# Performance work log

Measured on AMD Instinct MI355X. Metric: run time of the kernel, lower is better.

## Reference

```python
import jax, jax.numpy as jnp
import numpy as np

NEG_INF = jnp.finfo(jnp.float32).min

def setup_inputs() -> dict:
    key = jax.random.key(0)
    k1, k2, k3, k4 = jax.random.split(key, 4)
    B, H, S, DK, DV = 2, 16, 2048, 64, 64
    Q = jax.random.normal(k1, (B, H, S, DK), dtype=jnp.float32)
    K = jax.random.normal(k2, (B, H, S, DK), dtype=jnp.float32)
    V = jax.random.normal(k3, (B, H, S, DV), dtype=jnp.float32)
    mask = jax.random.randint(k4, (B, 1, S, S), 0, 2, dtype=jnp.int32)
    return {"Q": Q, "K": K, "V": V, "mask": mask}

def reference(Q, K, V, mask):
    d_k = Q.shape[-1]
    # scores: [B, H, Sq, Sk]
    scores = jnp.einsum('bhqd,bhkd->bhqk', Q, K) / jnp.sqrt(jnp.float32(d_k))
    scores = jnp.where(mask == 0, NEG_INF, scores)
    attn_weights = jax.nn.softmax(scores, axis=-1)
    # dropout p=0.0 -> identity (eval-mode reference)
    output = jnp.einsum('bhqk,bhkv->bhqv', attn_weights, V)
    return (output, attn_weights)
```

## Files before the change

### kernel.cpp

```cpp
#include <hip/hip_runtime.h>


typedef __attribute__((ext_vector_type(4))) float f32x4;
typedef __attribute__((ext_vector_type(8))) short s16x8;
typedef __attribute__((ext_vector_type(4))) unsigned short u16x4;
typedef __attribute__((ext_vector_type(8))) unsigned short u16x8;
typedef __attribute__((ext_vector_type(4))) unsigned int u32x4;

#define S_LEN 2048
#define D_DIM 64
#define H_NUM 16
#define B_NUM 2
#define NT    32
#define SW    32
#define QSCALE 0.18033688011112042f

__device__ __forceinline__ int swz(int row, int colByte) {
  return row * 128 + (colByte ^ ((row & 7) << 4));
}

__device__ __forceinline__ unsigned short f2bf(float f) {
  unsigned int x = __builtin_bit_cast(unsigned int, f);
  x = (x + 0x7FFFu + ((x >> 16) & 1u)) >> 16;
  return (unsigned short)x;
}

__device__ __forceinline__ unsigned cvt_pk_bf16(float lo, float hi) {
  unsigned r;
  asm("v_cvt_pk_bf16_f32 %0, %1, %2" : "=v"(r) : "v"(lo), "v"(hi));
  return r;
}

__device__ __forceinline__ f32x4 mfma16(f32x4 acc, s16x8 a, s16x8 b) {
  return __builtin_amdgcn_mfma_f32_16x16x32_bf16(a, b, acc, 0, 0, 0);
}


__global__ __launch_bounds__(256) void prep_kernel(
    const float* __restrict__ Q, const float* __restrict__ K,
    const float* __restrict__ V, const int* __restrict__ m,
    u16x4* __restrict__ Q16, u16x4* __restrict__ K16,
    unsigned short* __restrict__ VT, unsigned long long* __restrict__ bits)
{
  const int blk = blockIdx.x;
  const int tid = threadIdx.x;

  if (blk < 1024) {
    __shared__ unsigned short t[64][72];
    const int bh = blk >> 5;
    const int st = blk & 31;
    const float* src = V + ((size_t)bh * S_LEN + st * 64) * D_DIM;
    const int r0 = tid >> 4;
    const int c  = (tid & 15) * 4;
#pragma unroll
    for (int i = 0; i < 4; ++i) {
      const int r = r0 + i * 16;
      float4 v = *(const float4*)(src + r * D_DIM + c);
      t[c + 0][r] = f2bf(v.x); t[c + 1][r] = f2bf(v.y);
      t[c + 2][r] = f2bf(v.z); t[c + 3][r] = f2bf(v.w);
    }
    __syncthreads();
#pragma unroll
    for (int i = 0; i < 4; ++i) {
      const int idx = tid + i * 256;
      const int d  = idx >> 4;
      const int t0 = (idx & 15) * 4;
      const int sp = ((t0 >> 5) & 1) * 32 + ((t0 & 7) >> 2) * 16 + ((t0 >> 3) & 3) * 4;
      u16x4 o = *(const u16x4*)&t[d][sp];
      *(u16x4*)(VT + ((size_t)bh * D_DIM + d) * S_LEN + st * 64 + t0) = o;
    }
  } else if (blk < 2048) {
    const int n4 = B_NUM * H_NUM * S_LEN * D_DIM / 4;
    const int step = 1024 * 256;
    for (int i = (blk - 1024) * 256 + tid; i < n4; i += step) {
      float4 q = ((const float4*)Q)[i];
      Q16[i] = u16x4{f2bf(q.x * QSCALE), f2bf(q.y * QSCALE),
                     f2bf(q.z * QSCALE), f2bf(q.w * QSCALE)};
      float4 k = ((const float4*)K)[i];
      K16[i] = u16x4{f2bf(k.x), f2bf(k.y), f2bf(k.z), f2bf(k.w)};
    }
  } else {
    const int total = B_NUM * S_LEN * S_LEN;
    const int step  = 1024 * 256;
    for (int i = (blk - 2048) * 256 + tid; i < total; i += step) {
      unsigned long long b = __ballot(m[i] != 0);
      if ((tid & 63) == 0) bits[i >> 6] = b;
    }
  }
}


__global__ __launch_bounds__(256) void attn_rowsum_kernel(
    const unsigned short* __restrict__ Q16, const unsigned short* __restrict__ K16,
    const unsigned long long* __restrict__ Mb, float* __restrict__ lpq)
{
  const int tid  = threadIdx.x;
  const int lane = tid & 63;
  const int wv   = tid >> 6;
  const int l15  = lane & 15;
  const int g4   = lane >> 4;

  const int wg = blockIdx.x;
  const int lg = (wg & 7) * 128 + (wg >> 3);
  const int qt = lg & 31;
  const int bh = lg >> 5;
  const int b  = bh >> 4;

  __shared__ __align__(16) char Kbuf[16384];

  const unsigned short* Qg16 = Q16 + ((size_t)bh * S_LEN + qt * 64 + wv * 16 + l15) * D_DIM + g4 * 8;
  const unsigned short* Kg16 = K16 + (size_t)bh * S_LEN * D_DIM;
  float* lpg = lpq + (size_t)bh * S_LEN + qt * 64;
  const unsigned long long* Mg = Mb + ((size_t)b * S_LEN + qt * 64) * SW;

  const s16x8 qa0 = *(const s16x8*)Qg16;
  const s16x8 qa1 = *(const s16x8*)(Qg16 + 32);

  float lps = 0.f;

  const int sr  = tid >> 3;
  const int ss  = tid & 7;
  const int ssb = ss * 16;

  {
    u16x8 k0 = *(const u16x8*)(Kg16 + (size_t)sr * D_DIM + ss * 8);
    u16x8 k1 = *(const u16x8*)(Kg16 + (size_t)(sr + 32) * D_DIM + ss * 8);
    *(u16x8*)(Kbuf + swz(sr, ssb))      = k0;
    *(u16x8*)(Kbuf + swz(sr + 32, ssb)) = k1;
  }
  __syncthreads();

  int cur = 0;
  for (int kt = 0; kt < NT; ++kt) {
    const int ktn = (kt + 1 < NT) ? kt + 1 : kt;
    u16x8 kr0 = *(const u16x8*)(Kg16 + (size_t)(ktn * 64 + sr) * D_DIM + ss * 8);
    u16x8 kr1 = *(const u16x8*)(Kg16 + (size_t)(ktn * 64 + sr + 32) * D_DIM + ss * 8);
    __builtin_amdgcn_sched_barrier(0);

    char* Kc = Kbuf + cur * 8192;
    const unsigned long long mw = Mg[(wv * 16 + l15) * SW + kt];

    f32x4 sacc[4];
#pragma unroll
    for (int i = 0; i < 4; ++i) sacc[i] = f32x4{0.f, 0.f, 0.f, 0.f};
#pragma unroll
    for (int ct = 0; ct < 4; ++ct) {
      s16x8 b0 = *(const s16x8*)(Kc + swz(ct * 16 + l15, g4 * 16));
      s16x8 b1 = *(const s16x8*)(Kc + swz(ct * 16 + l15, g4 * 16 + 64));
      sacc[ct] = mfma16(sacc[ct], b0, qa0);
      sacc[ct] = mfma16(sacc[ct], b1, qa1);
    }

#pragma unroll
    for (int ct = 0; ct < 4; ++ct) {
#pragma unroll
      for (int r = 0; r < 4; ++r) {
        float e = __builtin_amdgcn_exp2f(sacc[ct][r]);
        lps += ((mw >> (ct * 16 + g4 * 4 + r)) & 1ull) ? e : 0.f;
      }
    }

    char* Kn = Kbuf + (cur ^ 1) * 8192;
    *(u16x8*)(Kn + swz(sr, ssb))      = kr0;
    *(u16x8*)(Kn + swz(sr + 32, ssb)) = kr1;
    __syncthreads();
    cur ^= 1;
  }

  lps += __shfl_xor(lps, 16);
  lps += __shfl_xor(lps, 32);
  if (g4 == 0) lpg[wv * 16 + l15] = 1.0f / lps;
}


__global__ __launch_bounds__(256) void attn_main_kernel(
    const unsigned short* __restrict__ Q16, const unsigned short* __restrict__ K16,
    const unsigned short* __restrict__ VT16, const unsigned long long* __restrict__ Mb,
    const float* __restrict__ lpq, float* __restrict__ Op, float* __restrict__ Wp)
{
  const int tid  = threadIdx.x;
  const int lane = tid & 63;
  const int wv   = tid >> 6;
  const int l15  = lane & 15;
  const int g4   = lane >> 4;

  const int wg = blockIdx.x;
  const int lg = (wg & 7) * 128 + (wg >> 3);
  const int qt = lg & 31;
  const int bh = lg >> 5;
  const int b  = bh >> 4;

  __shared__ __align__(16) char lds[32768];
  char* Kbuf = lds;
  char* Vbuf = lds + 16384;

  const unsigned short* Qg16 = Q16 + ((size_t)bh * S_LEN + qt * 64 + wv * 16 + l15) * D_DIM + g4 * 8;
  const unsigned short* Kg16 = K16 + (size_t)bh * S_LEN * D_DIM;
  const unsigned short* Vg   = VT16 + (size_t)bh * D_DIM * S_LEN;
  float* Og = Op + ((size_t)bh * S_LEN + qt * 64) * D_DIM;
  float* Wrow = Wp + ((size_t)bh * S_LEN + qt * 64 + wv * 16 + l15) * S_LEN;
  const unsigned long long* Mg = Mb + ((size_t)b * S_LEN + qt * 64) * SW;
  const float* lpg = lpq + (size_t)bh * S_LEN + qt * 64;

  const s16x8 qa0 = *(const s16x8*)Qg16;
  const s16x8 qa1 = *(const s16x8*)(Qg16 + 32);

  const float lpr = lpg[wv * 16 + l15];
  float lpn[4];
#pragma unroll
  for (int r = 0; r < 4; ++r) lpn[r] = lpg[wv * 16 + g4 * 4 + r];

  f32x4 oacc[4];
#pragma unroll
  for (int i = 0; i < 4; ++i) oacc[i] = f32x4{0.f, 0.f, 0.f, 0.f};

  const int sr  = tid >> 3;
  const int ss  = tid & 7;
  const int ssb = ss * 16;

  {
    u16x8 k0 = *(const u16x8*)(Kg16 + (size_t)sr * D_DIM + ss * 8);
    u16x8 k1 = *(const u16x8*)(Kg16 + (size_t)(sr + 32) * D_DIM + ss * 8);
    u16x8 v0 = *(const u16x8*)(Vg + (size_t)sr * S_LEN + ss * 8);
    u16x8 v1 = *(const u16x8*)(Vg + (size_t)(sr + 32) * S_LEN + ss * 8);
    *(u16x8*)(Kbuf + swz(sr, ssb))      = k0;
    *(u16x8*)(Kbuf + swz(sr + 32, ssb)) = k1;
    *(u16x8*)(Vbuf + swz(sr, ssb))      = v0;
    *(u16x8*)(Vbuf + swz(sr + 32, ssb)) = v1;
  }
  __syncthreads();

  int cur = 0;
  for (int kt = 0; kt < NT; ++kt) {
    const int ktn = (kt + 1 < NT) ? kt + 1 : kt;
    u16x8 kr0 = *(const u16x8*)(Kg16 + (size_t)(ktn * 64 + sr) * D_DIM + ss * 8);
    u16x8 kr1 = *(const u16x8*)(Kg16 + (size_t)(ktn * 64 + sr + 32) * D_DIM + ss * 8);
    u16x8 vr0 = *(const u16x8*)(Vg + (size_t)sr * S_LEN + ktn * 64 + ss * 8);
    u16x8 vr1 = *(const u16x8*)(Vg + (size_t)(sr + 32) * S_LEN + ktn * 64 + ss * 8);
    __builtin_amdgcn_sched_barrier(0);

    char* Kc = Kbuf + cur * 8192;
    char* Vc = Vbuf + cur * 8192;

    const unsigned long long mw = Mg[(wv * 16 + l15) * SW + kt];

    f32x4 sacc[4];
#pragma unroll
    for (int i = 0; i < 4; ++i) sacc[i] = f32x4{0.f, 0.f, 0.f, 0.f};
#pragma unroll
    for (int ct = 0; ct < 4; ++ct) {
      s16x8 b0 = *(const s16x8*)(Kc + swz(ct * 16 + l15, g4 * 16));
      s16x8 b1 = *(const s16x8*)(Kc + swz(ct * 16 + l15, g4 * 16 + 64));
      sacc[ct] = mfma16(sacc[ct], b0, qa0);
      sacc[ct] = mfma16(sacc[ct], b1, qa1);
    }

    unsigned pw[8];
#pragma unroll
    for (int ct = 0; ct < 4; ++ct) {
      float e0 = __builtin_amdgcn_exp2f(sacc[ct][0]);
      float e1 = __builtin_amdgcn_exp2f(sacc[ct][1]);
      float e2 = __builtin_amdgcn_exp2f(sacc[ct][2]);
      float e3 = __builtin_amdgcn_exp2f(sacc[ct][3]);
      e0 = ((mw >> (ct * 16 + g4 * 4 + 0)) & 1ull) ? e0 : 0.f;
      e1 = ((mw >> (ct * 16 + g4 * 4 + 1)) & 1ull) ? e1 : 0.f;
      e2 = ((mw >> (ct * 16 + g4 * 4 + 2)) & 1ull) ? e2 : 0.f;
      e3 = ((mw >> (ct * 16 + g4 * 4 + 3)) & 1ull) ? e3 : 0.f;
      f32x4 w = {e0 * lpr, e1 * lpr, e2 * lpr, e3 * lpr};
      __builtin_nontemporal_store(w,
          (f32x4*)(Wrow + (size_t)kt * 64 + ct * 16 + g4 * 4));
      pw[2 * ct]     = cvt_pk_bf16(e0, e1);
      pw[2 * ct + 1] = cvt_pk_bf16(e2, e3);
    }
    const s16x8 pa0 = __builtin_bit_cast(s16x8, u32x4{pw[0], pw[1], pw[2], pw[3]});
    const s16x8 pa1 = __builtin_bit_cast(s16x8, u32x4{pw[4], pw[5], pw[6], pw[7]});

#pragma unroll
    for (int ct = 0; ct < 4; ++ct) {
      s16x8 v0 = *(const s16x8*)(Vc + swz(ct * 16 + l15, g4 * 16));
      s16x8 v1 = *(const s16x8*)(Vc + swz(ct * 16 + l15, g4 * 16 + 64));
      oacc[ct] = mfma16(oacc[ct], pa0, v0);
      oacc[ct] = mfma16(oacc[ct], pa1, v1);
    }

    char* Kn = Kbuf + (cur ^ 1) * 8192;
    char* Vn = Vbuf + (cur ^ 1) * 8192;
    *(u16x8*)(Kn + swz(sr, ssb))      = kr0;
    *(u16x8*)(Kn + swz(sr + 32, ssb)) = kr1;
    *(u16x8*)(Vn + swz(sr, ssb))      = vr0;
    *(u16x8*)(Vn + swz(sr + 32, ssb)) = vr1;
    __syncthreads();
    cur ^= 1;
  }

#pragma unroll
  for (int ct = 0; ct < 4; ++ct)
#pragma unroll
    for (int r = 0; r < 4; ++r)
      Og[(size_t)(wv * 16 + g4 * 4 + r) * D_DIM + ct * 16 + l15] = oacc[ct][r] * lpn[r];
}


__global__ __launch_bounds__(256) void attn_fwd_kernel(
    const float* __restrict__ Qp, const float* __restrict__ Kp, const float* __restrict__ Vp,
    const int* __restrict__ Mi, float* __restrict__ Op, float* __restrict__ Wp)
{
  const int tid  = threadIdx.x;
  const int lane = tid & 63;
  const int wv   = tid >> 6;
  const int l15  = lane & 15;
  const int g4   = lane >> 4;

  const int wg = blockIdx.x;
  const int lg = (wg & 7) * 128 + (wg >> 3);
  const int qt = lg & 31;
  const int bh = lg >> 5;
  const int b  = bh >> 4;

  __shared__ __align__(16) char lds[32768];
  char* Qs  = lds;
  char* Ks  = lds + 8192;
  char* VTs = lds + 16384;
  char* Ps  = lds + 24576 + (wv << 11);

  const float* Qg = Qp + ((size_t)bh * S_LEN + qt * 64) * D_DIM;
  const float* Kg = Kp + (size_t)bh * S_LEN * D_DIM;
  const float* Vg = Vp + (size_t)bh * S_LEN * D_DIM;
  float* Og = Op + ((size_t)bh * S_LEN + qt * 64) * D_DIM;
  float* Wg = Wp + ((size_t)bh * S_LEN + qt * 64) * S_LEN;
  const int* Mig = Mi + ((size_t)b * S_LEN + qt * 64) * S_LEN;

  {
    const int r0 = tid >> 4;
    const int c  = (tid & 15) * 4;
#pragma unroll
    for (int i = 0; i < 4; ++i) {
      const int r = r0 + i * 16;
      float4 v = *(const float4*)(Qg + r * D_DIM + c);
      ushort4 p; p.x = f2bf(v.x); p.y = f2bf(v.y); p.z = f2bf(v.z); p.w = f2bf(v.w);
      *(ushort4*)(Qs + swz(r, c * 2)) = p;
    }
  }
  __syncthreads();
  const s16x8 qa0 = *(const s16x8*)(Qs + swz(wv * 16 + l15, g4 * 16));
  const s16x8 qa1 = *(const s16x8*)(Qs + swz(wv * 16 + l15, g4 * 16 + 64));

  f32x4 oacc[4];
#pragma unroll
  for (int i = 0; i < 4; ++i) oacc[i] = f32x4{0.f, 0.f, 0.f, 0.f};
  float lp[4] = {0.f, 0.f, 0.f, 0.f};

  const int qrow = wv * 16 + g4 * 4;

  for (int kt = 0; kt < NT; ++kt) {
    __syncthreads();
    {
      const int r0 = tid >> 4;
      const int c  = (tid & 15) * 4;
      const float* Kt = Kg + kt * 64 * D_DIM;
#pragma unroll
      for (int i = 0; i < 4; ++i) {
        const int r = r0 + i * 16;
        float4 v = *(const float4*)(Kt + r * D_DIM + c);
        ushort4 p; p.x = f2bf(v.x); p.y = f2bf(v.y); p.z = f2bf(v.z); p.w = f2bf(v.w);
        *(ushort4*)(Ks + swz(r, c * 2)) = p;
      }
      const float* Vt = Vg + kt * 64 * D_DIM;
#pragma unroll
      for (int i = 0; i < 2; ++i) {
        const int rr = (tid >> 4) * 2 + i * 32;
        float4 a  = *(const float4*)(Vt + rr * D_DIM + c);
        float4 bq = *(const float4*)(Vt + (rr + 1) * D_DIM + c);
        const float av[4] = {a.x, a.y, a.z, a.w};
        const float bv[4] = {bq.x, bq.y, bq.z, bq.w};
#pragma unroll
        for (int j = 0; j < 4; ++j) {
          unsigned pk = (unsigned)f2bf(av[j]) | ((unsigned)f2bf(bv[j]) << 16);
          *(unsigned*)(VTs + swz(c + j, rr * 2)) = pk;
        }
      }
    }
    __syncthreads();

    f32x4 sacc[4];
#pragma unroll
    for (int i = 0; i < 4; ++i) sacc[i] = f32x4{0.f, 0.f, 0.f, 0.f};
#pragma unroll
    for (int ct = 0; ct < 4; ++ct) {
      s16x8 b0 = *(const s16x8*)(Ks + swz(ct * 16 + l15, g4 * 16));
      s16x8 b1 = *(const s16x8*)(Ks + swz(ct * 16 + l15, g4 * 16 + 64));
      sacc[ct] = mfma16(sacc[ct], qa0, b0);
      sacc[ct] = mfma16(sacc[ct], qa1, b1);
    }

#pragma unroll
    for (int ct = 0; ct < 4; ++ct) {
#pragma unroll
      for (int r = 0; r < 4; ++r) {
        float e = __expf(sacc[ct][r] * 0.125f);
        bool keep = Mig[(size_t)(qrow + r) * S_LEN + kt * 64 + ct * 16 + l15] != 0;
        e = keep ? e : 0.f;
        lp[r] += e;
        *(unsigned short*)(Ps + swz(g4 * 4 + r, (ct * 16 + l15) * 2)) = f2bf(e);
      }
    }
    asm volatile("s_waitcnt lgkmcnt(0)" ::: "memory");
    __builtin_amdgcn_sched_barrier(0);

    const s16x8 pa0 = *(const s16x8*)(Ps + swz(l15, g4 * 16));
    const s16x8 pa1 = *(const s16x8*)(Ps + swz(l15, g4 * 16 + 64));
#pragma unroll
    for (int ct = 0; ct < 4; ++ct) {
      s16x8 v0 = *(const s16x8*)(VTs + swz(ct * 16 + l15, g4 * 16));
      s16x8 v1 = *(const s16x8*)(VTs + swz(ct * 16 + l15, g4 * 16 + 64));
      oacc[ct] = mfma16(oacc[ct], pa0, v0);
      oacc[ct] = mfma16(oacc[ct], pa1, v1);
    }
  }

#pragma unroll
  for (int r = 0; r < 4; ++r) {
    float v = lp[r];
    v += __shfl_xor(v, 1);
    v += __shfl_xor(v, 2);
    v += __shfl_xor(v, 4);
    v += __shfl_xor(v, 8);
    lp[r] = 1.0f / v;
  }

#pragma unroll
  for (int ct = 0; ct < 4; ++ct)
#pragma unroll
    for (int r = 0; r < 4; ++r)
      Og[(size_t)(qrow + r) * D_DIM + ct * 16 + l15] = oacc[ct][r] * lp[r];

  for (int kt = 0; kt < NT; ++kt) {
    __syncthreads();
    {
      const int r0 = tid >> 4;
      const int c  = (tid & 15) * 4;
      const float* Kt = Kg + kt * 64 * D_DIM;
#pragma unroll
      for (int i = 0; i < 4; ++i) {
        const int r = r0 + i * 16;
        float4 v = *(const float4*)(Kt + r * D_DIM + c);
        ushort4 p; p.x = f2bf(v.x); p.y = f2bf(v.y); p.z = f2bf(v.z); p.w = f2bf(v.w);
        *(ushort4*)(Ks + swz(r, c * 2)) = p;
      }
    }
    __syncthreads();

    f32x4 sacc[4];
#pragma unroll
    for (int i = 0; i < 4; ++i) sacc[i] = f32x4{0.f, 0.f, 0.f, 0.f};
#pragma unroll
    for (int ct = 0; ct < 4; ++ct) {
      s16x8 b0 = *(const s16x8*)(Ks + swz(ct * 16 + l15, g4 * 16));
      s16x8 b1 = *(const s16x8*)(Ks + swz(ct * 16 + l15, g4 * 16 + 64));
      sacc[ct] = mfma16(sacc[ct], qa0, b0);
      sacc[ct] = mfma16(sacc[ct], qa1, b1);
    }

#pragma unroll
    for (int ct = 0; ct < 4; ++ct) {
#pragma unroll
      for (int r = 0; r < 4; ++r) {
        float e = __expf(sacc[ct][r] * 0.125f);
        bool keep = Mig[(size_t)(qrow + r) * S_LEN + kt * 64 + ct * 16 + l15] != 0;
        e = keep ? e : 0.f;
        __builtin_nontemporal_store(e * lp[r],
            Wg + (size_t)(qrow + r) * S_LEN + kt * 64 + ct * 16 + l15);
      }
    }
  }
}

extern "C" void kernel_launch(void* const* d_in, const int* in_sizes, int n_in,
                              void* d_out, int out_size, void* d_ws, size_t ws_size,
                              hipStream_t stream) {
  (void)in_sizes; (void)n_in; (void)out_size;
  const float* Q   = (const float*)d_in[0];
  const float* K   = (const float*)d_in[1];
  const float* V   = (const float*)d_in[2];
  const int* mask  = (const int*)d_in[3];
  float* Out = (float*)d_out;
  float* W   = Out + (size_t)B_NUM * H_NUM * S_LEN * D_DIM;

  const size_t bits_bytes = (size_t)(B_NUM * S_LEN * S_LEN / 64) * 8;
  const size_t t16_bytes  = (size_t)B_NUM * H_NUM * S_LEN * D_DIM * 2;
  const size_t lp_bytes   = (size_t)B_NUM * H_NUM * S_LEN * 4;
  unsigned long long* bits = (unsigned long long*)d_ws;

  if (ws_size >= bits_bytes + 3 * t16_bytes + lp_bytes) {
    unsigned short* Q16 = (unsigned short*)((char*)d_ws + bits_bytes);
    unsigned short* K16 = Q16 + t16_bytes / 2;
    unsigned short* VT  = K16 + t16_bytes / 2;
    float* lpq = (float*)((char*)d_ws + bits_bytes + 3 * t16_bytes);
    prep_kernel<<<3072, 256, 0, stream>>>(Q, K, V, mask,
                                          (u16x4*)Q16, (u16x4*)K16, VT, bits);
    attn_rowsum_kernel<<<1024, 256, 0, stream>>>(Q16, K16, bits, lpq);
    attn_main_kernel<<<1024, 256, 0, stream>>>(Q16, K16, VT, bits, lpq, Out, W);
  } else {
    attn_fwd_kernel<<<1024, 256, 0, stream>>>(Q, K, V, mask, Out, W);
  }
}
```

Before: 230.2 us.

## Share K/V tiles across two query tiles with 512-thread blocks in main kernel

```diff
diff --git a/kernel.cpp b/kernel.cpp
--- a/kernel.cpp
+++ b/kernel.cpp
@@ -173,7 +173,7 @@
 }
 
 
-__global__ __launch_bounds__(256) void attn_main_kernel(
+__global__ __launch_bounds__(512, 4) void attn_main_kernel(
     const unsigned short* __restrict__ Q16, const unsigned short* __restrict__ K16,
     const unsigned short* __restrict__ VT16, const unsigned long long* __restrict__ Mb,
     const float* __restrict__ lpq, float* __restrict__ Op, float* __restrict__ Wp)
@@ -183,32 +183,34 @@
   const int wv   = tid >> 6;
   const int l15  = lane & 15;
   const int g4   = lane >> 4;
+  const int wt   = wv & 3;
 
   const int wg = blockIdx.x;
-  const int lg = (wg & 7) * 128 + (wg >> 3);
-  const int qt = lg & 31;
-  const int bh = lg >> 5;
+  const int lg = (wg & 7) * 64 + (wg >> 3);
+  const int tp = lg & 15;
+  const int bh = lg >> 4;
   const int b  = bh >> 4;
+  const int qt = tp * 2 + (wv >> 2);
 
   __shared__ __align__(16) char lds[32768];
   char* Kbuf = lds;
   char* Vbuf = lds + 16384;
 
-  const unsigned short* Qg16 = Q16 + ((size_t)bh * S_LEN + qt * 64 + wv * 16 + l15) * D_DIM + g4 * 8;
+  const unsigned short* Qg16 = Q16 + ((size_t)bh * S_LEN + qt * 64 + wt * 16 + l15) * D_DIM + g4 * 8;
   const unsigned short* Kg16 = K16 + (size_t)bh * S_LEN * D_DIM;
   const unsigned short* Vg   = VT16 + (size_t)bh * D_DIM * S_LEN;
   float* Og = Op + ((size_t)bh * S_LEN + qt * 64) * D_DIM;
-  float* Wrow = Wp + ((size_t)bh * S_LEN + qt * 64 + wv * 16 + l15) * S_LEN;
-  const unsigned long long* Mg = Mb + ((size_t)b * S_LEN + qt * 64) * SW;
+  float* Wrow = Wp + ((size_t)bh * S_LEN + qt * 64 + wt * 16 + l15) * S_LEN;
+  const unsigned long long* Mrow = Mb + ((size_t)b * S_LEN + qt * 64 + wt * 16 + l15) * SW;
   const float* lpg = lpq + (size_t)bh * S_LEN + qt * 64;
 
   const s16x8 qa0 = *(const s16x8*)Qg16;
   const s16x8 qa1 = *(const s16x8*)(Qg16 + 32);
 
-  const float lpr = lpg[wv * 16 + l15];
+  const float lpr = lpg[wt * 16 + l15];
   float lpn[4];
 #pragma unroll
-  for (int r = 0; r < 4; ++r) lpn[r] = lpg[wv * 16 + g4 * 4 + r];
+  for (int r = 0; r < 4; ++r) lpn[r] = lpg[wt * 16 + g4 * 4 + r];
 
   f32x4 oacc[4];
 #pragma unroll
@@ -220,29 +222,23 @@
 
   {
     u16x8 k0 = *(const u16x8*)(Kg16 + (size_t)sr * D_DIM + ss * 8);
-    u16x8 k1 = *(const u16x8*)(Kg16 + (size_t)(sr + 32) * D_DIM + ss * 8);
     u16x8 v0 = *(const u16x8*)(Vg + (size_t)sr * S_LEN + ss * 8);
-    u16x8 v1 = *(const u16x8*)(Vg + (size_t)(sr + 32) * S_LEN + ss * 8);
-    *(u16x8*)(Kbuf + swz(sr, ssb))      = k0;
-    *(u16x8*)(Kbuf + swz(sr + 32, ssb)) = k1;
-    *(u16x8*)(Vbuf + swz(sr, ssb))      = v0;
-    *(u16x8*)(Vbuf + swz(sr + 32, ssb)) = v1;
+    *(u16x8*)(Kbuf + swz(sr, ssb)) = k0;
+    *(u16x8*)(Vbuf + swz(sr, ssb)) = v0;
   }
   __syncthreads();
 
   int cur = 0;
   for (int kt = 0; kt < NT; ++kt) {
     const int ktn = (kt + 1 < NT) ? kt + 1 : kt;
-    u16x8 kr0 = *(const u16x8*)(Kg16 + (size_t)(ktn * 64 + sr) * D_DIM + ss * 8);
-    u16x8 kr1 = *(const u16x8*)(Kg16 + (size_t)(ktn * 64 + sr + 32) * D_DIM + ss * 8);
-    u16x8 vr0 = *(const u16x8*)(Vg + (size_t)sr * S_LEN + ktn * 64 + ss * 8);
-    u16x8 vr1 = *(const u16x8*)(Vg + (size_t)(sr + 32) * S_LEN + ktn * 64 + ss * 8);
+    u16x8 kr = *(const u16x8*)(Kg16 + (size_t)(ktn * 64 + sr) * D_DIM + ss * 8);
+    u16x8 vr = *(const u16x8*)(Vg + (size_t)sr * S_LEN + ktn * 64 + ss * 8);
     __builtin_amdgcn_sched_barrier(0);
 
     char* Kc = Kbuf + cur * 8192;
     char* Vc = Vbuf + cur * 8192;
 
-    const unsigned long long mw = Mg[(wv * 16 + l15) * SW + kt];
+    const unsigned long long mw = Mrow[kt];
 
     f32x4 sacc[4];
 #pragma unroll
@@ -285,10 +281,8 @@
 
     char* Kn = Kbuf + (cur ^ 1) * 8192;
     char* Vn = Vbuf + (cur ^ 1) * 8192;
-    *(u16x8*)(Kn + swz(sr, ssb))      = kr0;
-    *(u16x8*)(Kn + swz(sr + 32, ssb)) = kr1;
-    *(u16x8*)(Vn + swz(sr, ssb))      = vr0;
-    *(u16x8*)(Vn + swz(sr + 32, ssb)) = vr1;
+    *(u16x8*)(Kn + swz(sr, ssb)) = kr;
+    *(u16x8*)(Vn + swz(sr, ssb)) = vr;
     __syncthreads();
     cur ^= 1;
   }
@@ -297,7 +291,7 @@
   for (int ct = 0; ct < 4; ++ct)
 #pragma unroll
     for (int r = 0; r < 4; ++r)
-      Og[(size_t)(wv * 16 + g4 * 4 + r) * D_DIM + ct * 16 + l15] = oacc[ct][r] * lpn[r];
+      Og[(size_t)(wt * 16 + g4 * 4 + r) * D_DIM + ct * 16 + l15] = oacc[ct][r] * lpn[r];
 }
 
 
@@ -499,7 +493,7 @@
     prep_kernel<<<3072, 256, 0, stream>>>(Q, K, V, mask,
                                           (u16x4*)Q16, (u16x4*)K16, VT, bits);
     attn_rowsum_kernel<<<1024, 256, 0, stream>>>(Q16, K16, bits, lpq);
-    attn_main_kernel<<<1024, 256, 0, stream>>>(Q16, K16, VT, bits, lpq, Out, W);
+    attn_main_kernel<<<512, 512, 0, stream>>>(Q16, K16, VT, bits, lpq, Out, W);
   } else {
     attn_fwd_kernel<<<1024, 256, 0, stream>>>(Q, K, V, mask, Out, W);
   }
```

After: 241.0 us. +4.7%, slower.
